# Kernel tuning notes

Hardware: AMD Instinct MI355X
Metric: run time of the kernel (lower is better)

Reference implementation:

```python
import jax, jax.numpy as jnp
import numpy as np
import math

INPUT_SIZE = 512
HIDDEN = 1024
OUTPUT = 512


def _uniform(key, shape, stdv):
    return jax.random.uniform(key, shape, jnp.float32, -stdv, stdv)


def setup_inputs() -> dict:
    key = jax.random.key(0)
    ks = jax.random.split(key, 11)
    stdv = 1.0 / math.sqrt(HIDDEN)
    x = jax.random.normal(ks[0], (128, 512, INPUT_SIZE), jnp.float32)
    return {
        "x": x,
        "w_ih1": _uniform(ks[1], (4 * HIDDEN, INPUT_SIZE), stdv),
        "w_hh1": _uniform(ks[2], (4 * HIDDEN, HIDDEN), stdv),
        "b_ih1": _uniform(ks[3], (4 * HIDDEN,), stdv),
        "b_hh1": _uniform(ks[4], (4 * HIDDEN,), stdv),
        "w_ih2": _uniform(ks[5], (4 * HIDDEN, HIDDEN), stdv),
        "w_hh2": _uniform(ks[6], (4 * HIDDEN, HIDDEN), stdv),
        "b_ih2": _uniform(ks[7], (4 * HIDDEN,), stdv),
        "b_hh2": _uniform(ks[8], (4 * HIDDEN,), stdv),
        "w_out": _uniform(ks[9], (OUTPUT, HIDDEN), 1.0 / math.sqrt(HIDDEN)),
        "b_out": _uniform(ks[10], (OUTPUT,), 1.0 / math.sqrt(HIDDEN)),
    }


def _cell(x_t, h, c, w_ih, w_hh, b_ih, b_hh):
    # gates: [B, 4H], chunk order: i, f, g, o (matches torch chunk(4, 1))
    gates = x_t @ w_ih.T + b_ih + h @ w_hh.T + b_hh
    i, f, g, o = jnp.split(gates, 4, axis=1)
    i = jax.nn.sigmoid(i)
    f = jax.nn.sigmoid(f)
    g = jnp.tanh(g)
    o = jax.nn.sigmoid(o)
    c_new = f * c + i * g
    h_new = o * jnp.tanh(c_new)
    return h_new, c_new


def reference(x, w_ih1, w_hh1, b_ih1, b_hh1, w_ih2, w_hh2, b_ih2, b_hh2, w_out, b_out):
    B = x.shape[0]
    H = w_hh1.shape[1]
    zeros = jnp.zeros((B, H), x.dtype)

    def step(carry, x_t):
        h1, c1, h2, c2 = carry
        h1, c1 = _cell(x_t, h1, c1, w_ih1, w_hh1, b_ih1, b_hh1)
        h2, c2 = _cell(h1, h2, c2, w_ih2, w_hh2, b_ih2, b_hh2)
        return (h1, c1, h2, c2), None

    xs = jnp.swapaxes(x, 0, 1)  # [T, B, D]
    (h1, c1, h2, c2), _ = jax.lax.scan(step, (zeros, zeros, zeros, zeros), xs)
    return h2 @ w_out.T + b_out
```

## Files before the change

kernel.cpp:

```cpp
#include <hip/hip_runtime.h>
#include <hip/hip_bf16.h>
#include <math.h>

typedef __bf16 bf16;
typedef __bf16 bf16x8 __attribute__((ext_vector_type(8)));
typedef float f32x16 __attribute__((ext_vector_type(16)));

#define T_STEPS 512
#define BATCH   128
#define DIN     512
#define HID     1024
#define G4      4096
#define DOUT    512

__device__ __forceinline__ float sigm(float x){ return 1.0f / (1.0f + __expf(-x)); }

__device__ __forceinline__ int zoff(int b, int k){
    return (k >> 5) * 4096 + ((k >> 4) & 1) * 2048 + (b >> 5) * 512 +
           ((k >> 3) & 1) * 256 + (b & 31) * 8 + (k & 7);
}

#define GLOAD_LDS(gsrc, ldsdst) \
  __builtin_amdgcn_global_load_lds((const __attribute__((address_space(1))) void*)(gsrc), \
                                   (__attribute__((address_space(3))) void*)(ldsdst), 16, 0, 0)


__global__ void wstage(const float* __restrict__ src, bf16* __restrict__ hi,
                       bf16* __restrict__ lo, int lk){
    int i = blockIdx.x * 256 + threadIdx.x;
    int K = 1 << lk;
    int n = i >> lk, k = i & (K - 1);
    float v = src[i];
    bf16 h = (bf16)v;
    int off = ((n >> 7) * (K >> 5) + (k >> 5)) * 4096 + ((k >> 4) & 1) * 2048 +
              ((n >> 5) & 3) * 512 + ((k >> 3) & 1) * 256 + (n & 31) * 8 + (k & 7);
    hi[off] = h;
    lo[off] = (bf16)(v - (float)h);
}

__global__ void xstage(const float* __restrict__ x, bf16* __restrict__ hi,
                       bf16* __restrict__ lo){
    int i = blockIdx.x * 256 + threadIdx.x;
    int d = i & 511;
    int b = (i >> 9) & 127;
    int t = i >> 16;
    float v = x[((size_t)b * T_STEPS + t) * DIN + d];
    bf16 h = (bf16)v;
    size_t off = (size_t)t * 65536 + zoff(b, d);
    hi[off] = h;
    lo[off] = (bf16)(v - (float)h);
}

__global__ void bias_kernel(const float* __restrict__ bih1, const float* __restrict__ bhh1,
                            const float* __restrict__ bih2, const float* __restrict__ bhh2,
                            float* __restrict__ bias1, float* __restrict__ bias2){
    int i = blockIdx.x * 256 + threadIdx.x;
    if (i < G4){
        bias1[i] = bih1[i] + bhh1[i];
        bias2[i] = bih2[i] + bhh2[i];
    }
}

__global__ __launch_bounds__(256)
void gemm_step(const bf16* __restrict__ x_h,  const bf16* __restrict__ x_l,
               const bf16* __restrict__ h1_h, const bf16* __restrict__ h1_l,
               const bf16* __restrict__ h2_h, const bf16* __restrict__ h2_l,
               const bf16* __restrict__ w1x_h, const bf16* __restrict__ w1x_l,
               const bf16* __restrict__ w1h_h, const bf16* __restrict__ w1h_l,
               const bf16* __restrict__ w2i_h, const bf16* __restrict__ w2i_l,
               const bf16* __restrict__ w2h_h, const bf16* __restrict__ w2h_l,
               float* __restrict__ gpart, int t)
{
    int g     = blockIdx.x >> 5;
    int ntile = blockIdx.x & 31;
    if (t == T_STEPS && g < 3) return;
    if (t == 0 && g >= 3)      return;
    int p1 = (t - 1) & 1, p2 = t & 1;

    const bf16 *Ah, *Al, *Wh, *Wl;
    int kstep0, wks;
    switch (g){
      case 0: Ah = x_h + (size_t)t * 65536; Al = x_l + (size_t)t * 65536;
              Wh = w1x_h; Wl = w1x_l; kstep0 = 0;  wks = 16; break;
      case 1: Ah = h1_h + p1 * 131072; Al = h1_l + p1 * 131072;
              Wh = w1h_h; Wl = w1h_l; kstep0 = 0;  wks = 32; break;
      case 2: Ah = h1_h + p1 * 131072; Al = h1_l + p1 * 131072;
              Wh = w1h_h; Wl = w1h_l; kstep0 = 16; wks = 32; break;
      case 3: Ah = h1_h + p1 * 131072; Al = h1_l + p1 * 131072;
              Wh = w2i_h; Wl = w2i_l; kstep0 = 0;  wks = 32; break;
      case 4: Ah = h1_h + p1 * 131072; Al = h1_l + p1 * 131072;
              Wh = w2i_h; Wl = w2i_l; kstep0 = 16; wks = 32; break;
      case 5: Ah = h2_h + p2 * 131072; Al = h2_l + p2 * 131072;
              Wh = w2h_h; Wl = w2h_l; kstep0 = 0;  wks = 32; break;
      default: Ah = h2_h + p2 * 131072; Al = h2_l + p2 * 131072;
              Wh = w2h_h; Wl = w2h_l; kstep0 = 16; wks = 32; break;
    }

    __shared__ __align__(1024) char smem[65536];
    int wave = threadIdx.x >> 6, lane = threadIdx.x & 63;
    int wm = wave >> 1, wn = wave & 1;
    int laneoff = ((lane >> 5) << 9) + ((lane & 31) << 4);

    auto stage = [&](int buf, int s){
        int ks = kstep0 + s;
        const bf16* Ash = Ah + (size_t)ks * 4096;
        const bf16* Asl = Al + (size_t)ks * 4096;
        const bf16* Wsh = Wh + ((size_t)ntile * wks + ks) * 4096;
        const bf16* Wsl = Wl + ((size_t)ntile * wks + ks) * 4096;
        char* base = smem + buf * 32768;
        #pragma unroll
        for (int c = 0; c < 2; ++c){
            int ii = wave * 2 + c;
            GLOAD_LDS(Ash + ii * 512 + lane * 8, base          + ii * 1024);
            GLOAD_LDS(Asl + ii * 512 + lane * 8, base + 8192   + ii * 1024);
            GLOAD_LDS(Wsh + ii * 512 + lane * 8, base + 16384  + ii * 1024);
            GLOAD_LDS(Wsl + ii * 512 + lane * 8, base + 24576  + ii * 1024);
        }
    };

    f32x16 a00 = {0,0,0,0,0,0,0,0,0,0,0,0,0,0,0,0};
    f32x16 a01 = a00, a10 = a00, a11 = a00;

    stage(0, 0);
    __syncthreads();
    for (int s = 0; s < 16; ++s){
        if (s < 15) stage((s + 1) & 1, s + 1);
        const char* b = smem + (s & 1) * 32768;
        #pragma unroll
        for (int k2 = 0; k2 < 2; ++k2){
            bf16x8 ah0 = *(const bf16x8*)(b + k2*4096 + (wm*2    )*1024 + laneoff);
            bf16x8 ah1 = *(const bf16x8*)(b + k2*4096 + (wm*2 + 1)*1024 + laneoff);
            bf16x8 al0 = *(const bf16x8*)(b + 8192  + k2*4096 + (wm*2    )*1024 + laneoff);
            bf16x8 al1 = *(const bf16x8*)(b + 8192  + k2*4096 + (wm*2 + 1)*1024 + laneoff);
            bf16x8 wh0 = *(const bf16x8*)(b + 16384 + k2*4096 + (wn*2    )*1024 + laneoff);
            bf16x8 wh1 = *(const bf16x8*)(b + 16384 + k2*4096 + (wn*2 + 1)*1024 + laneoff);
            bf16x8 wl0 = *(const bf16x8*)(b + 24576 + k2*4096 + (wn*2    )*1024 + laneoff);
            bf16x8 wl1 = *(const bf16x8*)(b + 24576 + k2*4096 + (wn*2 + 1)*1024 + laneoff);
            a00 = __builtin_amdgcn_mfma_f32_32x32x16_bf16(ah0, wh0, a00, 0, 0, 0);
            a01 = __builtin_amdgcn_mfma_f32_32x32x16_bf16(ah0, wh1, a01, 0, 0, 0);
            a10 = __builtin_amdgcn_mfma_f32_32x32x16_bf16(ah1, wh0, a10, 0, 0, 0);
            a11 = __builtin_amdgcn_mfma_f32_32x32x16_bf16(ah1, wh1, a11, 0, 0, 0);
            a00 = __builtin_amdgcn_mfma_f32_32x32x16_bf16(ah0, wl0, a00, 0, 0, 0);
            a01 = __builtin_amdgcn_mfma_f32_32x32x16_bf16(ah0, wl1, a01, 0, 0, 0);
            a10 = __builtin_amdgcn_mfma_f32_32x32x16_bf16(ah1, wl0, a10, 0, 0, 0);
            a11 = __builtin_amdgcn_mfma_f32_32x32x16_bf16(ah1, wl1, a11, 0, 0, 0);
            a00 = __builtin_amdgcn_mfma_f32_32x32x16_bf16(al0, wh0, a00, 0, 0, 0);
            a01 = __builtin_amdgcn_mfma_f32_32x32x16_bf16(al0, wh1, a01, 0, 0, 0);
            a10 = __builtin_amdgcn_mfma_f32_32x32x16_bf16(al1, wh0, a10, 0, 0, 0);
            a11 = __builtin_amdgcn_mfma_f32_32x32x16_bf16(al1, wh1, a11, 0, 0, 0);
        }
        __syncthreads();
    }

    float* gp = gpart + (size_t)g * (BATCH * G4);
    int col0 = ntile * 128 + (wn * 2    ) * 32 + (lane & 31);
    int col1 = ntile * 128 + (wn * 2 + 1) * 32 + (lane & 31);
    #pragma unroll
    for (int r = 0; r < 16; ++r){
        int row32 = (r & 3) + 8 * (r >> 2) + 4 * (lane >> 5);
        gp[(size_t)(wm * 64 + row32) * G4 + col0]      = a00[r];
        gp[(size_t)(wm * 64 + row32) * G4 + col1]      = a01[r];
        gp[(size_t)(wm * 64 + 32 + row32) * G4 + col0] = a10[r];
        gp[(size_t)(wm * 64 + 32 + row32) * G4 + col1] = a11[r];
    }
}

__global__ __launch_bounds__(256)
void cell_step(const float* __restrict__ gpart,
               const float* __restrict__ bias1, const float* __restrict__ bias2,
               float* __restrict__ c1, float* __restrict__ c2,
               bf16* __restrict__ h1_h, bf16* __restrict__ h1_l,
               bf16* __restrict__ h2_h, bf16* __restrict__ h2_l,
               float* __restrict__ h2t, int t)
{
    int tid = blockIdx.x * 256 + threadIdx.x;
    for (int L = 0; L < 2; ++L){
        if (L == 0 && t == T_STEPS) continue;
        if (L == 1 && t == 0)       continue;
        int s = L ? (t - 1) : t;
        int p = s & 1;
        const float* bias = L ? bias2 : bias1;
        float* c  = L ? c2 : c1;
        bf16* hh = (L ? h2_h : h1_h) + p * 131072;
        bf16* hl = (L ? h2_l : h1_l) + p * 131072;
        int sh0 = L ? 3 : 0;
        int nsh = L ? 4 : 3;
        for (int it = tid; it < BATCH * HID; it += 65536){
            int b = it >> 10;
            int j = it & (HID - 1);
            size_t base = (size_t)b * G4 + j;
            float g4[4];
            #pragma unroll
            for (int q = 0; q < 4; ++q){
                float v = bias[j + q * 1024];
                for (int sh = 0; sh < nsh; ++sh)
                    v += gpart[(size_t)(sh0 + sh) * (BATCH * G4) + base + q * 1024];
                g4[q] = v;
            }
            float iv = sigm(g4[0]), fv = sigm(g4[1]), gv = tanhf(g4[2]), ov = sigm(g4[3]);
            float cn = fv * c[it] + iv * gv;
            c[it] = cn;
            float h = ov * tanhf(cn);
            bf16 hb = (bf16)h;
            int off = zoff(b, j);
            hh[off] = hb;
            hl[off] = (bf16)(h - (float)hb);
            if (L == 1 && s == T_STEPS - 1) h2t[(size_t)j * BATCH + b] = h;
        }
    }
}

__global__ __launch_bounds__(128)
void outproj(const float* __restrict__ h2t, const float* __restrict__ wout,
             const float* __restrict__ bout, float* __restrict__ out){
    int o = blockIdx.x;
    int b = threadIdx.x;
    float acc = bout[o];
    const float* wr = wout + (size_t)o * HID;
    for (int k = 0; k < HID; ++k)
        acc += wr[k] * h2t[(size_t)k * BATCH + b];
    out[(size_t)b * DOUT + o] = acc;
}

extern "C" void kernel_launch(void* const* d_in, const int* in_sizes, int n_in,
                              void* d_out, int out_size, void* d_ws, size_t ws_size,
                              hipStream_t stream)
{
    const float* x    = (const float*)d_in[0];
    const float* wih1 = (const float*)d_in[1];
    const float* whh1 = (const float*)d_in[2];
    const float* bih1 = (const float*)d_in[3];
    const float* bhh1 = (const float*)d_in[4];
    const float* wih2 = (const float*)d_in[5];
    const float* whh2 = (const float*)d_in[6];
    const float* bih2 = (const float*)d_in[7];
    const float* bhh2 = (const float*)d_in[8];
    const float* wout = (const float*)d_in[9];
    const float* bout = (const float*)d_in[10];
    float* out = (float*)d_out;

    char* p = (char*)d_ws;
    auto alloc = [&](size_t bytes) -> char* {
        char* r = p;
        p += (bytes + 1023) & ~(size_t)1023;
        return r;
    };

    bf16* x_h   = (bf16*)alloc((size_t)T_STEPS * 65536 * 2);
    bf16* x_l   = (bf16*)alloc((size_t)T_STEPS * 65536 * 2);
    bf16* w1x_h = (bf16*)alloc((size_t)G4 * DIN * 2);
    bf16* w1x_l = (bf16*)alloc((size_t)G4 * DIN * 2);
    bf16* w1h_h = (bf16*)alloc((size_t)G4 * HID * 2);
    bf16* w1h_l = (bf16*)alloc((size_t)G4 * HID * 2);
    bf16* w2i_h = (bf16*)alloc((size_t)G4 * HID * 2);
    bf16* w2i_l = (bf16*)alloc((size_t)G4 * HID * 2);
    bf16* w2h_h = (bf16*)alloc((size_t)G4 * HID * 2);
    bf16* w2h_l = (bf16*)alloc((size_t)G4 * HID * 2);
    float* bias1 = (float*)alloc(G4 * 4);
    float* bias2 = (float*)alloc(G4 * 4);
    char* zbase = p;
    bf16* h1_h = (bf16*)alloc((size_t)2 * 131072 * 2);
    bf16* h1_l = (bf16*)alloc((size_t)2 * 131072 * 2);
    bf16* h2_h = (bf16*)alloc((size_t)2 * 131072 * 2);
    bf16* h2_l = (bf16*)alloc((size_t)2 * 131072 * 2);
    float* c1  = (float*)alloc((size_t)BATCH * HID * 4);
    float* c2  = (float*)alloc((size_t)BATCH * HID * 4);
    size_t zbytes = (size_t)(p - zbase);
    float* gpart = (float*)alloc((size_t)7 * BATCH * G4 * 4);
    float* h2t   = (float*)alloc((size_t)HID * BATCH * 4);
    (void)ws_size; (void)in_sizes; (void)n_in; (void)out_size;

    wstage<<<(G4 * DIN) / 256, 256, 0, stream>>>(wih1, w1x_h, w1x_l, 9);
    wstage<<<(G4 * HID) / 256, 256, 0, stream>>>(whh1, w1h_h, w1h_l, 10);
    wstage<<<(G4 * HID) / 256, 256, 0, stream>>>(wih2, w2i_h, w2i_l, 10);
    wstage<<<(G4 * HID) / 256, 256, 0, stream>>>(whh2, w2h_h, w2h_l, 10);
    bias_kernel<<<(G4 + 255) / 256, 256, 0, stream>>>(bih1, bhh1, bih2, bhh2, bias1, bias2);
    xstage<<<(T_STEPS * BATCH * DIN) / 256, 256, 0, stream>>>(x, x_h, x_l);
    hipMemsetAsync(zbase, 0, zbytes, stream);

    for (int t = 0; t <= T_STEPS; ++t){
        gemm_step<<<224, 256, 0, stream>>>(x_h, x_l, h1_h, h1_l, h2_h, h2_l,
                                           w1x_h, w1x_l, w1h_h, w1h_l,
                                           w2i_h, w2i_l, w2h_h, w2h_l, gpart, t);
        cell_step<<<256, 256, 0, stream>>>(gpart, bias1, bias2, c1, c2,
                                           h1_h, h1_l, h2_h, h2_l, h2t, t);
    }

    outproj<<<DOUT, BATCH, 0, stream>>>(h2t, wout, bout, out);
}
```

Baseline: 13.26 ms.

## Fuse per-step GEMM and cell kernels into one persistent kernel with grid barriers

Replaces the 1026 per-timestep kernel launches with a single persistent kernel of 256 blocks that loops over time. A software grid barrier built on atomics separates the GEMM phase from the cell-update phase. Cell state and biases are now held in registers instead of global memory. This removes per-launch overhead and the c1/c2 global traffic, at the cost of two system-scope atomic barriers per step and reliance on all 256 blocks being resident at the same time.

New measurement: 47.52 ms. 3.58x slower.

```diff
diff --git a/kernel.cpp b/kernel.cpp
--- a/kernel.cpp
+++ b/kernel.cpp
@@ -61,152 +61,179 @@
     }
 }
 
-__global__ __launch_bounds__(256)
-void gemm_step(const bf16* __restrict__ x_h,  const bf16* __restrict__ x_l,
-               const bf16* __restrict__ h1_h, const bf16* __restrict__ h1_l,
-               const bf16* __restrict__ h2_h, const bf16* __restrict__ h2_l,
-               const bf16* __restrict__ w1x_h, const bf16* __restrict__ w1x_l,
-               const bf16* __restrict__ w1h_h, const bf16* __restrict__ w1h_l,
-               const bf16* __restrict__ w2i_h, const bf16* __restrict__ w2i_l,
-               const bf16* __restrict__ w2h_h, const bf16* __restrict__ w2h_l,
-               float* __restrict__ gpart, int t)
+__global__ __launch_bounds__(256, 1)
+void lstm_persist(const bf16* __restrict__ x_h, const bf16* __restrict__ x_l,
+                  bf16* __restrict__ h1_h, bf16* __restrict__ h1_l,
+                  bf16* __restrict__ h2_h, bf16* __restrict__ h2_l,
+                  const bf16* __restrict__ w1x_h, const bf16* __restrict__ w1x_l,
+                  const bf16* __restrict__ w1h_h, const bf16* __restrict__ w1h_l,
+                  const bf16* __restrict__ w2i_h, const bf16* __restrict__ w2i_l,
+                  const bf16* __restrict__ w2h_h, const bf16* __restrict__ w2h_l,
+                  const float* __restrict__ bias1, const float* __restrict__ bias2,
+                  float* __restrict__ gpart, float* __restrict__ h2t,
+                  unsigned* bar)
 {
-    int g     = blockIdx.x >> 5;
-    int ntile = blockIdx.x & 31;
-    if (t == T_STEPS && g < 3) return;
-    if (t == 0 && g >= 3)      return;
-    int p1 = (t - 1) & 1, p2 = t & 1;
-
-    const bf16 *Ah, *Al, *Wh, *Wl;
-    int kstep0, wks;
-    switch (g){
-      case 0: Ah = x_h + (size_t)t * 65536; Al = x_l + (size_t)t * 65536;
-              Wh = w1x_h; Wl = w1x_l; kstep0 = 0;  wks = 16; break;
-      case 1: Ah = h1_h + p1 * 131072; Al = h1_l + p1 * 131072;
-              Wh = w1h_h; Wl = w1h_l; kstep0 = 0;  wks = 32; break;
-      case 2: Ah = h1_h + p1 * 131072; Al = h1_l + p1 * 131072;
-              Wh = w1h_h; Wl = w1h_l; kstep0 = 16; wks = 32; break;
-      case 3: Ah = h1_h + p1 * 131072; Al = h1_l + p1 * 131072;
-              Wh = w2i_h; Wl = w2i_l; kstep0 = 0;  wks = 32; break;
-      case 4: Ah = h1_h + p1 * 131072; Al = h1_l + p1 * 131072;
-              Wh = w2i_h; Wl = w2i_l; kstep0 = 16; wks = 32; break;
-      case 5: Ah = h2_h + p2 * 131072; Al = h2_l + p2 * 131072;
-              Wh = w2h_h; Wl = w2h_l; kstep0 = 0;  wks = 32; break;
-      default: Ah = h2_h + p2 * 131072; Al = h2_l + p2 * 131072;
-              Wh = w2h_h; Wl = w2h_l; kstep0 = 16; wks = 32; break;
+    __shared__ __align__(1024) char smem[65536];
+    const int tid  = threadIdx.x;
+    const int wave = tid >> 6, lane = tid & 63;
+    const int wm = wave >> 1, wn = wave & 1;
+    const int bid = blockIdx.x;
+    const bool isG = bid < 224;
+    const int g = bid >> 5, ntile = bid & 31;
+    const int gtid = bid * 256 + tid;
+    const int laneoff = ((lane >> 5) << 9) + ((lane & 31) << 4);
+
+    float creg[2][2] = {{0.f, 0.f}, {0.f, 0.f}};
+    float breg[2][2][4];
+    #pragma unroll
+    for (int L = 0; L < 2; ++L){
+        const float* bias = L ? bias2 : bias1;
+        #pragma unroll
+        for (int u = 0; u < 2; ++u){
+            int j = (gtid + u * 65536) & 1023;
+            #pragma unroll
+            for (int q = 0; q < 4; ++q) breg[L][u][q] = bias[j + q * 1024];
+        }
     }
 
-    __shared__ __align__(1024) char smem[65536];
-    int wave = threadIdx.x >> 6, lane = threadIdx.x & 63;
-    int wm = wave >> 1, wn = wave & 1;
-    int laneoff = ((lane >> 5) << 9) + ((lane & 31) << 4);
-
-    auto stage = [&](int buf, int s){
-        int ks = kstep0 + s;
-        const bf16* Ash = Ah + (size_t)ks * 4096;
-        const bf16* Asl = Al + (size_t)ks * 4096;
-        const bf16* Wsh = Wh + ((size_t)ntile * wks + ks) * 4096;
-        const bf16* Wsl = Wl + ((size_t)ntile * wks + ks) * 4096;
-        char* base = smem + buf * 32768;
-        #pragma unroll
-        for (int c = 0; c < 2; ++c){
-            int ii = wave * 2 + c;
-            GLOAD_LDS(Ash + ii * 512 + lane * 8, base          + ii * 1024);
-            GLOAD_LDS(Asl + ii * 512 + lane * 8, base + 8192   + ii * 1024);
-            GLOAD_LDS(Wsh + ii * 512 + lane * 8, base + 16384  + ii * 1024);
-            GLOAD_LDS(Wsl + ii * 512 + lane * 8, base + 24576  + ii * 1024);
-        }
-    };
-
-    f32x16 a00 = {0,0,0,0,0,0,0,0,0,0,0,0,0,0,0,0};
-    f32x16 a01 = a00, a10 = a00, a11 = a00;
-
-    stage(0, 0);
-    __syncthreads();
-    for (int s = 0; s < 16; ++s){
-        if (s < 15) stage((s + 1) & 1, s + 1);
-        const char* b = smem + (s & 1) * 32768;
-        #pragma unroll
-        for (int k2 = 0; k2 < 2; ++k2){
-            bf16x8 ah0 = *(const bf16x8*)(b + k2*4096 + (wm*2    )*1024 + laneoff);
-            bf16x8 ah1 = *(const bf16x8*)(b + k2*4096 + (wm*2 + 1)*1024 + laneoff);
-            bf16x8 al0 = *(const bf16x8*)(b + 8192  + k2*4096 + (wm*2    )*1024 + laneoff);
-            bf16x8 al1 = *(const bf16x8*)(b + 8192  + k2*4096 + (wm*2 + 1)*1024 + laneoff);
-            bf16x8 wh0 = *(const bf16x8*)(b + 16384 + k2*4096 + (wn*2    )*1024 + laneoff);
-            bf16x8 wh1 = *(const bf16x8*)(b + 16384 + k2*4096 + (wn*2 + 1)*1024 + laneoff);
-            bf16x8 wl0 = *(const bf16x8*)(b + 24576 + k2*4096 + (wn*2    )*1024 + laneoff);
-            bf16x8 wl1 = *(const bf16x8*)(b + 24576 + k2*4096 + (wn*2 + 1)*1024 + laneoff);
-            a00 = __builtin_amdgcn_mfma_f32_32x32x16_bf16(ah0, wh0, a00, 0, 0, 0);
-            a01 = __builtin_amdgcn_mfma_f32_32x32x16_bf16(ah0, wh1, a01, 0, 0, 0);
-            a10 = __builtin_amdgcn_mfma_f32_32x32x16_bf16(ah1, wh0, a10, 0, 0, 0);
-            a11 = __builtin_amdgcn_mfma_f32_32x32x16_bf16(ah1, wh1, a11, 0, 0, 0);
-            a00 = __builtin_amdgcn_mfma_f32_32x32x16_bf16(ah0, wl0, a00, 0, 0, 0);
-            a01 = __builtin_amdgcn_mfma_f32_32x32x16_bf16(ah0, wl1, a01, 0, 0, 0);
-            a10 = __builtin_amdgcn_mfma_f32_32x32x16_bf16(ah1, wl0, a10, 0, 0, 0);
-            a11 = __builtin_amdgcn_mfma_f32_32x32x16_bf16(ah1, wl1, a11, 0, 0, 0);
-            a00 = __builtin_amdgcn_mfma_f32_32x32x16_bf16(al0, wh0, a00, 0, 0, 0);
-            a01 = __builtin_amdgcn_mfma_f32_32x32x16_bf16(al0, wh1, a01, 0, 0, 0);
-            a10 = __builtin_amdgcn_mfma_f32_32x32x16_bf16(al1, wh0, a10, 0, 0, 0);
-            a11 = __builtin_amdgcn_mfma_f32_32x32x16_bf16(al1, wh1, a11, 0, 0, 0);
+    unsigned target = 0;
+    auto gridbar = [&](){
+        target += 256;
+        __syncthreads();
+        if (tid == 0){
+            __threadfence_system();
+            __hip_atomic_fetch_add(bar, 1u, __ATOMIC_RELEASE, __HIP_MEMORY_SCOPE_SYSTEM);
+            while (__hip_atomic_load(bar, __ATOMIC_ACQUIRE, __HIP_MEMORY_SCOPE_SYSTEM) < target)
+                __builtin_amdgcn_s_sleep(2);
+            __threadfence_system();
         }
         __syncthreads();
-    }
-
-    float* gp = gpart + (size_t)g * (BATCH * G4);
-    int col0 = ntile * 128 + (wn * 2    ) * 32 + (lane & 31);
-    int col1 = ntile * 128 + (wn * 2 + 1) * 32 + (lane & 31);
-    #pragma unroll
-    for (int r = 0; r < 16; ++r){
-        int row32 = (r & 3) + 8 * (r >> 2) + 4 * (lane >> 5);
-        gp[(size_t)(wm * 64 + row32) * G4 + col0]      = a00[r];
-        gp[(size_t)(wm * 64 + row32) * G4 + col1]      = a01[r];
-        gp[(size_t)(wm * 64 + 32 + row32) * G4 + col0] = a10[r];
-        gp[(size_t)(wm * 64 + 32 + row32) * G4 + col1] = a11[r];
-    }
-}
-
-__global__ __launch_bounds__(256)
-void cell_step(const float* __restrict__ gpart,
-               const float* __restrict__ bias1, const float* __restrict__ bias2,
-               float* __restrict__ c1, float* __restrict__ c2,
-               bf16* __restrict__ h1_h, bf16* __restrict__ h1_l,
-               bf16* __restrict__ h2_h, bf16* __restrict__ h2_l,
-               float* __restrict__ h2t, int t)
-{
-    int tid = blockIdx.x * 256 + threadIdx.x;
-    for (int L = 0; L < 2; ++L){
-        if (L == 0 && t == T_STEPS) continue;
-        if (L == 1 && t == 0)       continue;
-        int s = L ? (t - 1) : t;
-        int p = s & 1;
-        const float* bias = L ? bias2 : bias1;
-        float* c  = L ? c2 : c1;
-        bf16* hh = (L ? h2_h : h1_h) + p * 131072;
-        bf16* hl = (L ? h2_l : h1_l) + p * 131072;
-        int sh0 = L ? 3 : 0;
-        int nsh = L ? 4 : 3;
-        for (int it = tid; it < BATCH * HID; it += 65536){
-            int b = it >> 10;
-            int j = it & (HID - 1);
-            size_t base = (size_t)b * G4 + j;
-            float g4[4];
+    };
+
+    for (int t = 0; t <= T_STEPS; ++t){
+        bool act = isG && !(t == T_STEPS && g < 3) && !(t == 0 && g >= 3);
+        if (act){
+            int p1 = (t - 1) & 1, p2 = t & 1;
+            const bf16 *Ah, *Al, *Wh, *Wl;
+            int kstep0, wks;
+            switch (g){
+              case 0: Ah = x_h + (size_t)t * 65536; Al = x_l + (size_t)t * 65536;
+                      Wh = w1x_h; Wl = w1x_l; kstep0 = 0;  wks = 16; break;
+              case 1: Ah = h1_h + p1 * 131072; Al = h1_l + p1 * 131072;
+                      Wh = w1h_h; Wl = w1h_l; kstep0 = 0;  wks = 32; break;
+              case 2: Ah = h1_h + p1 * 131072; Al = h1_l + p1 * 131072;
+                      Wh = w1h_h; Wl = w1h_l; kstep0 = 16; wks = 32; break;
+              case 3: Ah = h1_h + p1 * 131072; Al = h1_l + p1 * 131072;
+                      Wh = w2i_h; Wl = w2i_l; kstep0 = 0;  wks = 32; break;
+              case 4: Ah = h1_h + p1 * 131072; Al = h1_l + p1 * 131072;
+                      Wh = w2i_h; Wl = w2i_l; kstep0 = 16; wks = 32; break;
+              case 5: Ah = h2_h + p2 * 131072; Al = h2_l + p2 * 131072;
+                      Wh = w2h_h; Wl = w2h_l; kstep0 = 0;  wks = 32; break;
+              default: Ah = h2_h + p2 * 131072; Al = h2_l + p2 * 131072;
+                      Wh = w2h_h; Wl = w2h_l; kstep0 = 16; wks = 32; break;
+            }
+
+            auto stage = [&](int buf, int s){
+                int ks = kstep0 + s;
+                const bf16* Ash = Ah + (size_t)ks * 4096;
+                const bf16* Asl = Al + (size_t)ks * 4096;
+                const bf16* Wsh = Wh + ((size_t)ntile * wks + ks) * 4096;
+                const bf16* Wsl = Wl + ((size_t)ntile * wks + ks) * 4096;
+                char* base = smem + buf * 32768;
+                #pragma unroll
+                for (int c = 0; c < 2; ++c){
+                    int ii = wave * 2 + c;
+                    GLOAD_LDS(Ash + ii * 512 + lane * 8, base          + ii * 1024);
+                    GLOAD_LDS(Asl + ii * 512 + lane * 8, base + 8192   + ii * 1024);
+                    GLOAD_LDS(Wsh + ii * 512 + lane * 8, base + 16384  + ii * 1024);
+                    GLOAD_LDS(Wsl + ii * 512 + lane * 8, base + 24576  + ii * 1024);
+                }
+            };
+
+            f32x16 a00 = {0,0,0,0,0,0,0,0,0,0,0,0,0,0,0,0};
+            f32x16 a01 = a00, a10 = a00, a11 = a00;
+
+            stage(0, 0);
+            __syncthreads();
+            for (int s = 0; s < 16; ++s){
+                if (s < 15) stage((s + 1) & 1, s + 1);
+                const char* b = smem + (s & 1) * 32768;
+                #pragma unroll
+                for (int k2 = 0; k2 < 2; ++k2){
+                    bf16x8 ah0 = *(const bf16x8*)(b + k2*4096 + (wm*2    )*1024 + laneoff);
+                    bf16x8 ah1 = *(const bf16x8*)(b + k2*4096 + (wm*2 + 1)*1024 + laneoff);
+                    bf16x8 al0 = *(const bf16x8*)(b + 8192  + k2*4096 + (wm*2    )*1024 + laneoff);
+                    bf16x8 al1 = *(const bf16x8*)(b + 8192  + k2*4096 + (wm*2 + 1)*1024 + laneoff);
+                    bf16x8 wh0 = *(const bf16x8*)(b + 16384 + k2*4096 + (wn*2    )*1024 + laneoff);
+                    bf16x8 wh1 = *(const bf16x8*)(b + 16384 + k2*4096 + (wn*2 + 1)*1024 + laneoff);
+                    bf16x8 wl0 = *(const bf16x8*)(b + 24576 + k2*4096 + (wn*2    )*1024 + laneoff);
+                    bf16x8 wl1 = *(const bf16x8*)(b + 24576 + k2*4096 + (wn*2 + 1)*1024 + laneoff);
+                    a00 = __builtin_amdgcn_mfma_f32_32x32x16_bf16(ah0, wh0, a00, 0, 0, 0);
+                    a01 = __builtin_amdgcn_mfma_f32_32x32x16_bf16(ah0, wh1, a01, 0, 0, 0);
+                    a10 = __builtin_amdgcn_mfma_f32_32x32x16_bf16(ah1, wh0, a10, 0, 0, 0);
+                    a11 = __builtin_amdgcn_mfma_f32_32x32x16_bf16(ah1, wh1, a11, 0, 0, 0);
+                    a00 = __builtin_amdgcn_mfma_f32_32x32x16_bf16(ah0, wl0, a00, 0, 0, 0);
+                    a01 = __builtin_amdgcn_mfma_f32_32x32x16_bf16(ah0, wl1, a01, 0, 0, 0);
+                    a10 = __builtin_amdgcn_mfma_f32_32x32x16_bf16(ah1, wl0, a10, 0, 0, 0);
+                    a11 = __builtin_amdgcn_mfma_f32_32x32x16_bf16(ah1, wl1, a11, 0, 0, 0);
+                    a00 = __builtin_amdgcn_mfma_f32_32x32x16_bf16(al0, wh0, a00, 0, 0, 0);
+                    a01 = __builtin_amdgcn_mfma_f32_32x32x16_bf16(al0, wh1, a01, 0, 0, 0);
+                    a10 = __builtin_amdgcn_mfma_f32_32x32x16_bf16(al1, wh0, a10, 0, 0, 0);
+                    a11 = __builtin_amdgcn_mfma_f32_32x32x16_bf16(al1, wh1, a11, 0, 0, 0);
+                }
+                __syncthreads();
+            }
+
+            float* gp = gpart + (size_t)g * (BATCH * G4);
+            int col0 = ntile * 128 + (wn * 2    ) * 32 + (lane & 31);
+            int col1 = ntile * 128 + (wn * 2 + 1) * 32 + (lane & 31);
             #pragma unroll
-            for (int q = 0; q < 4; ++q){
-                float v = bias[j + q * 1024];
-                for (int sh = 0; sh < nsh; ++sh)
-                    v += gpart[(size_t)(sh0 + sh) * (BATCH * G4) + base + q * 1024];
-                g4[q] = v;
+            for (int r = 0; r < 16; ++r){
+                int row32 = (r & 3) + 8 * (r >> 2) + 4 * (lane >> 5);
+                gp[(size_t)(wm * 64 + row32) * G4 + col0]      = a00[r];
+                gp[(size_t)(wm * 64 + row32) * G4 + col1]      = a01[r];
+                gp[(size_t)(wm * 64 + 32 + row32) * G4 + col0] = a10[r];
+                gp[(size_t)(wm * 64 + 32 + row32) * G4 + col1] = a11[r];
             }
-            float iv = sigm(g4[0]), fv = sigm(g4[1]), gv = tanhf(g4[2]), ov = sigm(g4[3]);
-            float cn = fv * c[it] + iv * gv;
-            c[it] = cn;
-            float h = ov * tanhf(cn);
-            bf16 hb = (bf16)h;
-            int off = zoff(b, j);
-            hh[off] = hb;
-            hl[off] = (bf16)(h - (float)hb);
-            if (L == 1 && s == T_STEPS - 1) h2t[(size_t)j * BATCH + b] = h;
         }
+        gridbar();
+
+        #pragma unroll
+        for (int L = 0; L < 2; ++L){
+            if (L == 0 && t == T_STEPS) continue;
+            if (L == 1 && t == 0)       continue;
+            int s = L ? (t - 1) : t;
+            int p = s & 1;
+            bf16* hh = (L ? h2_h : h1_h) + p * 131072;
+            bf16* hl = (L ? h2_l : h1_l) + p * 131072;
+            int sh0 = L ? 3 : 0;
+            int nsh = L ? 4 : 3;
+            #pragma unroll
+            for (int u = 0; u < 2; ++u){
+                int it = gtid + u * 65536;
+                int b = it >> 10;
+                int j = it & 1023;
+                size_t base = (size_t)b * G4 + j;
+                float g4[4];
+                #pragma unroll
+                for (int q = 0; q < 4; ++q){
+                    float v = breg[L][u][q];
+                    for (int sh = 0; sh < nsh; ++sh)
+                        v += gpart[(size_t)(sh0 + sh) * (BATCH * G4) + base + q * 1024];
+                    g4[q] = v;
+                }
+                float iv = sigm(g4[0]), fv = sigm(g4[1]), gv = tanhf(g4[2]), ov = sigm(g4[3]);
+                float cn = fv * creg[L][u] + iv * gv;
+                creg[L][u] = cn;
+                float h = ov * tanhf(cn);
+                bf16 hb = (bf16)h;
+                int off = zoff(b, j);
+                hh[off] = hb;
+                hl[off] = (bf16)(h - (float)hb);
+                if (L == 1 && s == T_STEPS - 1) h2t[(size_t)j * BATCH + b] = h;
+            }
+        }
+        gridbar();
     }
 }
 
@@ -263,8 +290,7 @@
     bf16* h1_l = (bf16*)alloc((size_t)2 * 131072 * 2);
     bf16* h2_h = (bf16*)alloc((size_t)2 * 131072 * 2);
     bf16* h2_l = (bf16*)alloc((size_t)2 * 131072 * 2);
-    float* c1  = (float*)alloc((size_t)BATCH * HID * 4);
-    float* c2  = (float*)alloc((size_t)BATCH * HID * 4);
+    unsigned* bar = (unsigned*)alloc(1024);
     size_t zbytes = (size_t)(p - zbase);
     float* gpart = (float*)alloc((size_t)7 * BATCH * G4 * 4);
     float* h2t   = (float*)alloc((size_t)HID * BATCH * 4);
@@ -278,13 +304,10 @@
     xstage<<<(T_STEPS * BATCH * DIN) / 256, 256, 0, stream>>>(x, x_h, x_l);
     hipMemsetAsync(zbase, 0, zbytes, stream);
 
-    for (int t = 0; t <= T_STEPS; ++t){
-        gemm_step<<<224, 256, 0, stream>>>(x_h, x_l, h1_h, h1_l, h2_h, h2_l,
-                                           w1x_h, w1x_l, w1h_h, w1h_l,
-                                           w2i_h, w2i_l, w2h_h, w2h_l, gpart, t);
-        cell_step<<<256, 256, 0, stream>>>(gpart, bias1, bias2, c1, c2,
-                                           h1_h, h1_l, h2_h, h2_l, h2t, t);
-    }
+    lstm_persist<<<256, 256, 0, stream>>>(x_h, x_l, h1_h, h1_l, h2_h, h2_l,
+                                          w1x_h, w1x_l, w1h_h, w1h_l,
+                                          w2i_h, w2i_l, w2h_h, w2h_l,
+                                          bias1, bias2, gpart, h2t, bar);
 
     outproj<<<DOUT, BATCH, 0, stream>>>(h2t, wout, bout, out);
 }
```
